# Performance work log

Measured on AMD Instinct MI355X. Metric: run time of the kernel, lower is better.

## Reference

```python
import jax, jax.numpy as jnp
from jax import lax
import numpy as np

B = 8192


def setup_inputs() -> dict:
    key = jax.random.key(0)
    ks = jax.random.split(key, 10)
    rn = lambda i, shape, s: jax.random.normal(ks[i], shape, jnp.float32) * s
    x = jax.random.normal(ks[0], (B, 1, 28, 28), jnp.float32)
    conv1_w = rn(1, (8, 1, 3, 3), 0.3)
    conv2_w = rn(2, (16, 8, 3, 3), 0.15)
    fc1_w = rn(3, (64, 16), 0.25)
    fc2_w = rn(4, (4, 64), 0.15)
    theta = jax.random.uniform(ks[5], (4,), jnp.float32, 0.0, 2.0 * np.pi)
    # RandomLayer (30 random gates) folded into one fixed 16x16 unitary via QR
    a = jax.random.normal(ks[6], (16, 16), jnp.float32)
    b = jax.random.normal(ks[7], (16, 16), jnp.float32)
    q, _ = jnp.linalg.qr((a + 1j * b).astype(jnp.complex64))
    return dict(
        x=x,
        conv1_w=conv1_w, conv1_b=jnp.zeros((8,), jnp.float32),
        conv2_w=conv2_w, conv2_b=jnp.zeros((16,), jnp.float32),
        fc1_w=fc1_w, fc1_b=jnp.zeros((64,), jnp.float32),
        fc2_w=fc2_w, fc2_b=jnp.zeros((4,), jnp.float32),
        norm_g=jnp.ones((4,), jnp.float32), norm_b=jnp.zeros((4,), jnp.float32),
        theta=theta,
        u_re=jnp.real(q).astype(jnp.float32), u_im=jnp.imag(q).astype(jnp.float32),
        qnorm_g=jnp.ones((4,), jnp.float32), qnorm_b=jnp.zeros((4,), jnp.float32),
    )


def _forward(x, conv1_w, conv1_b, conv2_w, conv2_b, fc1_w, fc1_b, fc2_w, fc2_b,
             norm_g, norm_b, theta, u_re, u_im, qnorm_g, qnorm_b):
    bsz = x.shape[0]
    cplx = jnp.complex64

    def conv(h, w, b):
        return lax.conv_general_dilated(h, w, (1, 1), [(1, 1), (1, 1)]) + b[None, :, None, None]

    def mpool(h):
        return lax.reduce_window(h, -jnp.inf, lax.max, (1, 1, 2, 2), (1, 1, 2, 2), 'VALID')

    h = mpool(jax.nn.relu(conv(x, conv1_w, conv1_b)))   # [B,8,14,14]
    h = mpool(jax.nn.relu(conv(h, conv2_w, conv2_b)))   # [B,16,7,7]
    pooled = h[:, :, :6, :6].mean((-1, -2))             # avg_pool2d(.,6) -> [B,16]
    f = jax.nn.relu(pooled @ fc1_w.T + fc1_b)
    out = f @ fc2_w.T + fc2_b                           # [B,4]

    def bn(v, g, b):  # BatchNorm1d, training mode (biased batch var), eps=1e-5
        m = v.mean(0)
        var = v.var(0)
        return g * (v - m) * lax.rsqrt(var + 1e-5) + b

    out = bn(out, norm_g, norm_b)

    # ---- 4-qubit state-vector simulation (wire 0 = most significant bit) ----
    def ry(t):
        c = jnp.cos(t / 2).astype(cplx); s = jnp.sin(t / 2).astype(cplx)
        return jnp.stack([jnp.stack([c, -s], -1), jnp.stack([s, c], -1)], -2)

    def rx(t):
        c = jnp.cos(t / 2).astype(cplx); s = (-1j) * jnp.sin(t / 2).astype(cplx)
        return jnp.stack([jnp.stack([c, s], -1), jnp.stack([s, c], -1)], -2)

    def rz(t):
        e = jnp.exp(-1j * t.astype(cplx) / 2); z = jnp.zeros_like(e)
        return jnp.stack([jnp.stack([e, z], -1), jnp.stack([z, jnp.conj(e)], -1)], -2)

    def ap1(st, U, w):  # apply 1-qubit gate U ([2,2] or [B,2,2]) on wire w
        s = jnp.moveaxis(st, 1 + w, 4)
        sub = 'bxyzi,bji->bxyzj' if U.ndim == 3 else 'bxyzi,ji->bxyzj'
        return jnp.moveaxis(jnp.einsum(sub, s, U), 4, 1 + w)

    def ap_ctrl(st, U, cw, tw):  # controlled-U: ctrl wire cw, target wire tw
        s = jnp.moveaxis(st, (1 + cw, 1 + tw), (3, 4))
        s1 = jnp.einsum('bxyi,ji->bxyj', s[..., 1, :], U)
        s = jnp.stack([s[..., 0, :], s1], axis=-2)
        return jnp.moveaxis(s, (3, 4), (1 + cw, 1 + tw))

    state = jnp.zeros((bsz, 16), cplx).at[:, 0].set(1.0).reshape(bsz, 2, 2, 2, 2)

    # encoder '4x4_ryzxy': RY,RZ,RX,RY rounds over wires 0-3 (4 features cycled)
    ang = jnp.tile(out, (1, 4))  # [B,16]
    enc = [ry] * 4 + [rz] * 4 + [rx] * 4 + [ry] * 4
    for k, fn in enumerate(enc):
        state = ap1(state, fn(ang[:, k]), k % 4)

    # RandomLayer as a fixed 16x16 unitary
    U = (u_re + 1j * u_im).astype(cplx)
    state = jnp.einsum('bi,ji->bj', state.reshape(bsz, 16), U).reshape(bsz, 2, 2, 2, 2)

    state = ap1(state, rx(theta[0]), 0)
    state = ap1(state, ry(theta[1]), 1)
    state = ap1(state, rz(theta[2]), 2)
    state = ap_ctrl(state, rx(theta[3]), 0, 3)
    H = (jnp.array([[1.0, 1.0], [1.0, -1.0]], jnp.float32) / np.float32(np.sqrt(2.0))).astype(cplx)
    SX = 0.5 * jnp.array([[1 + 1j, 1 - 1j], [1 - 1j, 1 + 1j]], cplx)
    X = jnp.array([[0.0, 1.0], [1.0, 0.0]], jnp.float32).astype(cplx)
    state = ap1(state, H, 3)
    state = ap1(state, SX, 2)
    state = ap_ctrl(state, X, 3, 0)

    sf = state.reshape(bsz, 16)
    probs = sf.real ** 2 + sf.imag ** 2                 # [B,16]
    bits = (np.arange(16)[:, None] >> np.arange(3, -1, -1)[None, :]) & 1
    signs = jnp.asarray(1.0 - 2.0 * bits, jnp.float32)  # [16,4] PauliZ eigenvalues per wire
    q_out = probs @ signs                               # [B,4] <Z_w>
    q_out = bn(q_out, qnorm_g, qnorm_b)
    return out + q_out


def reference(x, conv1_w, conv1_b, conv2_w, conv2_b, fc1_w, fc1_b, fc2_w, fc2_b,
              norm_g, norm_b, theta, u_re, u_im, qnorm_g, qnorm_b):
    return _forward(x, conv1_w, conv1_b, conv2_w, conv2_b, fc1_w, fc1_b, fc2_w, fc2_b,
                    norm_g, norm_b, theta, u_re, u_im, qnorm_g, qnorm_b)
```

## Files before the change

### kernel.cpp

```cpp
#include <hip/hip_runtime.h>
#include <math.h>


#define XS_S 34
#define H1_S 20
#define H1_P 280
#define H1I_OFF 9216
#define BT_OFF  13696
#define SMEM_SZ 16000

typedef _Float16 half8 __attribute__((ext_vector_type(8)));
typedef float v4f __attribute__((ext_vector_type(4)));

__device__ __forceinline__ unsigned pkf16(float a, float b) {
    _Float16 ha = (_Float16)a, hb = (_Float16)b;
    unsigned short ua = __builtin_bit_cast(unsigned short, ha);
    unsigned short ub = __builtin_bit_cast(unsigned short, hb);
    return ((unsigned)ub << 16) | (unsigned)ua;
}

__device__ __forceinline__ float2 cmul(float2 a, float2 b) {
    return make_float2(a.x * b.x - a.y * b.y, a.x * b.y + a.y * b.x);
}
__device__ __forceinline__ float2 cadd(float2 a, float2 b) {
    return make_float2(a.x + b.x, a.y + b.y);
}

__device__ __forceinline__ void apply_1q(const float2* src, float2* dst, int t,
                                         float2 g00, float2 g01, float2 g10, float2 g11, int p)
{
    int j = t >> 4, i = t & 15;
    int jb = (j >> p) & 1;
    int k0 = j & ~(1 << p);
    int k1 = j | (1 << p);
    float2 a0 = src[k0 * 16 + i], a1 = src[k1 * 16 + i];
    float2 r = jb ? cadd(cmul(g10, a0), cmul(g11, a1))
                  : cadd(cmul(g00, a0), cmul(g01, a1));
    dst[j * 16 + i] = r;
}

__device__ __forceinline__ void apply_ctrl(const float2* src, float2* dst, int t,
                                           float2 g00, float2 g01, float2 g10, float2 g11,
                                           int pc, int pt)
{
    int j = t >> 4, i = t & 15;
    float2 r;
    if (((j >> pc) & 1) == 0) {
        r = src[j * 16 + i];
    } else {
        int jb = (j >> pt) & 1;
        int k0 = j & ~(1 << pt);
        int k1 = j | (1 << pt);
        float2 a0 = src[k0 * 16 + i], a1 = src[k1 * 16 + i];
        r = jb ? cadd(cmul(g10, a0), cmul(g11, a1))
               : cadd(cmul(g00, a0), cmul(g01, a1));
    }
    dst[j * 16 + i] = r;
}

__global__ __launch_bounds__(256, 6) void k_cnn(
    const float* __restrict__ x,
    const float* __restrict__ w1, const float* __restrict__ b1,
    const float* __restrict__ w2, const float* __restrict__ b2,
    const float* __restrict__ fw1, const float* __restrict__ fb1,
    const float* __restrict__ fw2, const float* __restrict__ fb2,
    float* __restrict__ out_pre, unsigned int* __restrict__ counters)
{
    __shared__ __align__(16) char smem[SMEM_SZ];
    __shared__ float w1t[72];
    __shared__ float b1t[8], b2t[16];
    __shared__ float pool_s[16];

    const int t = threadIdx.x;
    const int b = blockIdx.x;
    const float* xg = x + b * 784;
    float* xs = (float*)smem;
    unsigned* h1u = (unsigned*)(smem + H1I_OFF);

    if (b == 0 && t < 2) counters[t] = 0u;
    if (t < 57) {
        if (t < 29) xs[t] = 0.f;
        else        xs[(t - 28) * XS_S] = 0.f;
    }
    if (t < 108) {
        int pl = t / 27, r = t % 27;
        if (r < 14) h1u[pl * H1_P + r] = 0u;
        else        h1u[pl * H1_P + (r - 13) * H1_S] = 0u;
    }
    if (t >= 64 && t < 136) {
        int i = t - 64;
        w1t[(i % 9) * 8 + (i / 9)] = w1[i];
    }
    if (t < 196) {
        float4 v = ((const float4*)xg)[t];
        int p = t * 4;
        int yy = p / 28, xx = p % 28;
        int base = (yy + 1) * XS_S + xx + 1;
        xs[base] = v.x; xs[base + 1] = v.y; xs[base + 2] = v.z; xs[base + 3] = v.w;
    }
    if (t < 8)  b1t[t] = b1[t];
    if (t < 16) b2t[t] = b2[t];
    __syncthreads();

    if (t < 169) {
        const int py = t / 13, px = t % 13;
        float patch[4][4];
        #pragma unroll
        for (int dr = 0; dr < 4; ++dr) {
            int base = (2 * py + dr) * XS_S + 2 * px;
            float2 a = *(const float2*)&xs[base];
            float2 c = *(const float2*)&xs[base + 2];
            patch[dr][0] = a.x; patch[dr][1] = a.y;
            patch[dr][2] = c.x; patch[dr][3] = c.y;
        }
        float acc[8][2][2];
        #pragma unroll
        for (int c = 0; c < 8; ++c)
            #pragma unroll
            for (int dy = 0; dy < 2; ++dy)
                #pragma unroll
                for (int dx = 0; dx < 2; ++dx) acc[c][dy][dx] = 0.f;
        #pragma unroll
        for (int k = 0; k < 9; ++k) {
            const int ky = k / 3, kx = k % 3;
            float4 wA = *(const float4*)&w1t[k * 8];
            float4 wB = *(const float4*)&w1t[k * 8 + 4];
            float w8[8] = {wA.x, wA.y, wA.z, wA.w, wB.x, wB.y, wB.z, wB.w};
            #pragma unroll
            for (int c = 0; c < 8; ++c)
                #pragma unroll
                for (int dy = 0; dy < 2; ++dy)
                    #pragma unroll
                    for (int dx = 0; dx < 2; ++dx)
                        acc[c][dy][dx] = fmaf(patch[dy + ky][dx + kx], w8[c], acc[c][dy][dx]);
        }
        float v8[8];
        #pragma unroll
        for (int c = 0; c < 8; ++c) {
            float m = fmaxf(fmaxf(acc[c][0][0], acc[c][0][1]),
                            fmaxf(acc[c][1][0], acc[c][1][1])) + b1t[c];
            v8[c] = fmaxf(m, 0.f);
        }
        const int ha = (py + 1) * H1_S + (px + 1);
        h1u[ha]             = pkf16(v8[0], v8[1]);
        h1u[H1_P + ha]      = pkf16(v8[2], v8[3]);
        h1u[2 * H1_P + ha]  = pkf16(v8[4], v8[5]);
        h1u[3 * H1_P + ha]  = pkf16(v8[6], v8[7]);
    } else if (t >= 192) {
        unsigned short* bt = (unsigned short*)(smem + BT_OFF);
        for (int i = t - 192; i < 1152; i += 64) {
            int oc = i / 72, r = i % 72, ic = r / 9, kidx = r % 9;
            _Float16 h = (_Float16)w2[i];
            bt[oc * 72 + kidx * 8 + ic] = __builtin_bit_cast(unsigned short, h);
        }
    }
    __syncthreads();

    const int wv_id = t >> 6, lane = t & 63, quad = lane >> 4, n = lane & 15;
    v4f acc0 = {0.f, 0.f, 0.f, 0.f}, acc1 = acc0, acc2 = acc0;
    if (wv_id < 3) {
        const half8 hz = {0, 0, 0, 0, 0, 0, 0, 0};
        half8 bfr[3];
        int koff[3];
        #pragma unroll
        for (int kc = 0; kc < 3; ++kc) {
            const int kidx = kc * 4 + quad;
            bfr[kc] = (kidx < 9)
                ? *(const half8*)(smem + BT_OFF + n * 144 + kc * 64 + quad * 16)
                : hz;
            koff[kc] = (kidx < 9) ? (kidx / 3) * H1_S + (kidx % 3) : 0;
        }
        #pragma unroll
        for (int g = 0; g < 3; ++g) {
            const int m = (wv_id * 3 + g) * 16 + n;
            const int y = m / 12, xx2 = m % 12;
            const int pbase = y * H1_S + xx2;
            v4f* accp = (g == 0) ? &acc0 : (g == 1) ? &acc1 : &acc2;
            #pragma unroll
            for (int kc = 0; kc < 3; ++kc) {
                const int kidx = kc * 4 + quad;
                half8 af;
                if (kidx < 9) {
                    const int a0 = pbase + koff[kc];
                    uint4 pw;
                    pw.x = h1u[a0];
                    pw.y = h1u[H1_P + a0];
                    pw.z = h1u[2 * H1_P + a0];
                    pw.w = h1u[3 * H1_P + a0];
                    af = __builtin_bit_cast(half8, pw);
                } else {
                    af = hz;
                }
                *accp = __builtin_amdgcn_mfma_f32_16x16x32_f16(af, bfr[kc], *accp, 0, 0, 0);
            }
        }
    }
    __syncthreads();

    float* h2p = (float*)smem;
    if (wv_id < 3) {
        const int posb = (wv_id * 3) * 16 + quad * 4;
        #pragma unroll
        for (int r = 0; r < 4; ++r) h2p[(posb + r) * 16 + n]      = acc0[r];
        #pragma unroll
        for (int r = 0; r < 4; ++r) h2p[(posb + 16 + r) * 16 + n] = acc1[r];
        #pragma unroll
        for (int r = 0; r < 4; ++r) h2p[(posb + 32 + r) * 16 + n] = acc2[r];
    }
    __syncthreads();

    if (t < 64) {
        const int oc = t >> 2, q = t & 3;
        const float bias = b2t[oc];
        float s = 0.f;
        #pragma unroll
        for (int r = 0; r < 9; ++r) {
            int idx = q * 9 + r;
            int pr = idx / 6, pc = idx % 6;
            int p00 = (2 * pr * 12 + 2 * pc) * 16 + oc;
            float m = fmaxf(fmaxf(h2p[p00], h2p[p00 + 16]),
                            fmaxf(h2p[p00 + 192], h2p[p00 + 208]));
            s += fmaxf(m + bias, 0.f);
        }
        s += __shfl_xor(s, 1);
        s += __shfl_xor(s, 2);
        if (q == 0) pool_s[oc] = s * (1.f / 36.f);
    }
    __syncthreads();

    if (t < 64) {
        const float4* f4 = (const float4*)(fw1 + t * 16);
        float4 wa = f4[0], wb = f4[1], wc = f4[2], wd = f4[3];
        float a1 = fb1[t];
        a1 = fmaf(pool_s[0],  wa.x, a1); a1 = fmaf(pool_s[1],  wa.y, a1);
        a1 = fmaf(pool_s[2],  wa.z, a1); a1 = fmaf(pool_s[3],  wa.w, a1);
        a1 = fmaf(pool_s[4],  wb.x, a1); a1 = fmaf(pool_s[5],  wb.y, a1);
        a1 = fmaf(pool_s[6],  wb.z, a1); a1 = fmaf(pool_s[7],  wb.w, a1);
        a1 = fmaf(pool_s[8],  wc.x, a1); a1 = fmaf(pool_s[9],  wc.y, a1);
        a1 = fmaf(pool_s[10], wc.z, a1); a1 = fmaf(pool_s[11], wc.w, a1);
        a1 = fmaf(pool_s[12], wd.x, a1); a1 = fmaf(pool_s[13], wd.y, a1);
        a1 = fmaf(pool_s[14], wd.z, a1); a1 = fmaf(pool_s[15], wd.w, a1);
        float f = fmaxf(a1, 0.f);
        float p0 = f * fw2[t];
        float p1 = f * fw2[64 + t];
        float p2 = f * fw2[128 + t];
        float p3 = f * fw2[192 + t];
        #pragma unroll
        for (int off = 32; off > 0; off >>= 1) {
            p0 += __shfl_down(p0, off);
            p1 += __shfl_down(p1, off);
            p2 += __shfl_down(p2, off);
            p3 += __shfl_down(p3, off);
        }
        if (t == 0) {
            ((float4*)out_pre)[b] = make_float4(p0 + fb2[0], p1 + fb2[1],
                                                p2 + fb2[2], p3 + fb2[3]);
        }
    }
}

__global__ __launch_bounds__(256) void k_tail(
    float* __restrict__ out_pre,
    const float* __restrict__ ng, const float* __restrict__ nb,
    const float* __restrict__ theta,
    const float* __restrict__ u_re, const float* __restrict__ u_im,
    const float* __restrict__ qg, const float* __restrict__ qb,
    float* __restrict__ bins1, float* __restrict__ bins2,
    unsigned int* __restrict__ counters)
{
    __shared__ float red[256];
    __shared__ float ss1[8], ss2[8];
    __shared__ float2 A[256], B[256], Ms[256];
    const int t = threadIdx.x;
    const int sidx = blockIdx.x * 256 + t;

    float4 o4 = ((const float4*)out_pre)[sidx];
    A[t] = make_float2(u_re[t], u_im[t]);
    float th0 = theta[0], th1 = theta[1], th2 = theta[2], th3 = theta[3];

    float vals[8] = {o4.x, o4.y, o4.z, o4.w,
                     o4.x * o4.x, o4.y * o4.y, o4.z * o4.z, o4.w * o4.w};
    #pragma unroll
    for (int off = 32; off > 0; off >>= 1)
        #pragma unroll
        for (int k = 0; k < 8; ++k) vals[k] += __shfl_down(vals[k], off);
    if ((t & 63) == 0) {
        int wid = t >> 6;
        #pragma unroll
        for (int k = 0; k < 8; ++k) red[wid * 8 + k] = vals[k];
    }
    __syncthreads();
    if (t < 8) {
        float s = red[t] + red[8 + t] + red[16 + t] + red[24 + t];
        __hip_atomic_store(&bins1[blockIdx.x * 8 + t], s,
                           __ATOMIC_RELEASE, __HIP_MEMORY_SCOPE_AGENT);
    }
    __syncthreads();
    if (t == 0) { __threadfence(); atomicAdd(&counters[0], 1u); }

    __syncthreads();
    float c0 = cosf(0.5f * th0), s0 = sinf(0.5f * th0);
    apply_1q(A, B, t, make_float2(c0, 0), make_float2(0, -s0),
                      make_float2(0, -s0), make_float2(c0, 0), 3);
    __syncthreads();
    float c1 = cosf(0.5f * th1), s1 = sinf(0.5f * th1);
    apply_1q(B, A, t, make_float2(c1, 0), make_float2(-s1, 0),
                      make_float2(s1, 0), make_float2(c1, 0), 2);
    __syncthreads();
    float c2 = cosf(0.5f * th2), s2 = sinf(0.5f * th2);
    apply_1q(A, B, t, make_float2(c2, -s2), make_float2(0, 0),
                      make_float2(0, 0), make_float2(c2, s2), 1);
    __syncthreads();
    float c3 = cosf(0.5f * th3), s3 = sinf(0.5f * th3);
    apply_ctrl(B, A, t, make_float2(c3, 0), make_float2(0, -s3),
                        make_float2(0, -s3), make_float2(c3, 0), 3, 0);
    __syncthreads();
    const float hh = 0.70710678118654752440f;
    apply_1q(A, B, t, make_float2(hh, 0), make_float2(hh, 0),
                      make_float2(hh, 0), make_float2(-hh, 0), 0);
    __syncthreads();
    apply_1q(B, A, t, make_float2(0.5f, 0.5f), make_float2(0.5f, -0.5f),
                      make_float2(0.5f, -0.5f), make_float2(0.5f, 0.5f), 1);
    __syncthreads();
    apply_ctrl(A, B, t, make_float2(0, 0), make_float2(1, 0),
                        make_float2(1, 0), make_float2(0, 0), 0, 3);
    __syncthreads();
    Ms[t] = B[t];

    if (t == 0) {
        while (__hip_atomic_load(&counters[0], __ATOMIC_ACQUIRE,
                                 __HIP_MEMORY_SCOPE_AGENT) < 32u)
            __builtin_amdgcn_s_sleep(4);
    }
    __syncthreads();
    red[t] = bins1[t];
    __syncthreads();
    if (t < 8) {
        float s = 0.f;
        for (int bb = 0; bb < 32; ++bb) s += red[bb * 8 + t];
        red[t] = s;
    }
    if (t < 4) {
        float mean = red[t] * (1.f / 8192.f);
        float var = red[4 + t] * (1.f / 8192.f) - mean * mean;
        float sc = ng[t] * rsqrtf(var + 1e-5f);
        ss1[t] = sc;
        ss1[4 + t] = nb[t] - mean * sc;
    }
    __syncthreads();

    float a[4];
    a[0] = fmaf(ss1[0], o4.x, ss1[4]);
    a[1] = fmaf(ss1[1], o4.y, ss1[5]);
    a[2] = fmaf(ss1[2], o4.z, ss1[6]);
    a[3] = fmaf(ss1[3], o4.w, ss1[7]);
    float2 v[4][2];
    #pragma unroll
    for (int w = 0; w < 4; ++w) {
        float s, c;
        __sincosf(0.5f * a[w], &s, &c);
        float2 v0 = make_float2(c * c, -c * s);
        float2 v1 = make_float2(s * c, s * s);
        float2 n0 = make_float2(c * v0.x + s * v1.y, c * v0.y - s * v1.x);
        float2 n1 = make_float2(s * v0.y + c * v1.x, -s * v0.x + c * v1.y);
        v[w][0] = make_float2(c * n0.x - s * n1.x, c * n0.y - s * n1.y);
        v[w][1] = make_float2(s * n0.x + c * n1.x, s * n0.y + c * n1.y);
    }
    float2 st[16];
    #pragma unroll
    for (int idx = 0; idx < 16; ++idx) {
        float2 p = cmul(v[0][(idx >> 3) & 1], v[1][(idx >> 2) & 1]);
        p = cmul(p, v[2][(idx >> 1) & 1]);
        st[idx] = cmul(p, v[3][idx & 1]);
    }
    float q[4] = {0.f, 0.f, 0.f, 0.f};
    #pragma unroll
    for (int j = 0; j < 16; ++j) {
        float2 acc = make_float2(0.f, 0.f);
        #pragma unroll
        for (int i = 0; i < 16; ++i) {
            float2 mm = Ms[j * 16 + i];
            acc.x = fmaf(mm.x, st[i].x, acc.x);
            acc.x = fmaf(-mm.y, st[i].y, acc.x);
            acc.y = fmaf(mm.x, st[i].y, acc.y);
            acc.y = fmaf(mm.y, st[i].x, acc.y);
        }
        float pr = acc.x * acc.x + acc.y * acc.y;
        q[0] += ((j >> 3) & 1) ? -pr : pr;
        q[1] += ((j >> 2) & 1) ? -pr : pr;
        q[2] += ((j >> 1) & 1) ? -pr : pr;
        q[3] += (j & 1) ? -pr : pr;
    }

    float vals2[8] = {q[0], q[1], q[2], q[3],
                      q[0] * q[0], q[1] * q[1], q[2] * q[2], q[3] * q[3]};
    #pragma unroll
    for (int off = 32; off > 0; off >>= 1)
        #pragma unroll
        for (int k = 0; k < 8; ++k) vals2[k] += __shfl_down(vals2[k], off);
    __syncthreads();
    if ((t & 63) == 0) {
        int wid = t >> 6;
        #pragma unroll
        for (int k = 0; k < 8; ++k) red[wid * 8 + k] = vals2[k];
    }
    __syncthreads();
    if (t < 8) {
        float s = red[t] + red[8 + t] + red[16 + t] + red[24 + t];
        __hip_atomic_store(&bins2[blockIdx.x * 8 + t], s,
                           __ATOMIC_RELEASE, __HIP_MEMORY_SCOPE_AGENT);
    }
    __syncthreads();
    if (t == 0) {
        __threadfence();
        atomicAdd(&counters[1], 1u);
        while (__hip_atomic_load(&counters[1], __ATOMIC_ACQUIRE,
                                 __HIP_MEMORY_SCOPE_AGENT) < 32u)
            __builtin_amdgcn_s_sleep(4);
    }
    __syncthreads();
    red[t] = bins2[t];
    __syncthreads();
    if (t < 8) {
        float s = 0.f;
        for (int bb = 0; bb < 32; ++bb) s += red[bb * 8 + t];
        red[t] = s;
    }
    if (t < 4) {
        float m2 = red[t] * (1.f / 8192.f);
        float v2 = red[4 + t] * (1.f / 8192.f) - m2 * m2;
        float sc = qg[t] * rsqrtf(v2 + 1e-5f);
        ss2[t] = sc;
        ss2[4 + t] = qb[t] - m2 * sc;
    }
    __syncthreads();

    float4 r;
    r.x = a[0] + fmaf(ss2[0], q[0], ss2[4]);
    r.y = a[1] + fmaf(ss2[1], q[1], ss2[5]);
    r.z = a[2] + fmaf(ss2[2], q[2], ss2[6]);
    r.w = a[3] + fmaf(ss2[3], q[3], ss2[7]);
    ((float4*)out_pre)[sidx] = r;
}

extern "C" void kernel_launch(void* const* d_in, const int* in_sizes, int n_in,
                              void* d_out, int out_size, void* d_ws, size_t ws_size,
                              hipStream_t stream)
{
    const float* x     = (const float*)d_in[0];
    const float* w1    = (const float*)d_in[1];
    const float* b1    = (const float*)d_in[2];
    const float* w2    = (const float*)d_in[3];
    const float* b2    = (const float*)d_in[4];
    const float* fw1   = (const float*)d_in[5];
    const float* fb1   = (const float*)d_in[6];
    const float* fw2   = (const float*)d_in[7];
    const float* fb2   = (const float*)d_in[8];
    const float* ng    = (const float*)d_in[9];
    const float* nb    = (const float*)d_in[10];
    const float* theta = (const float*)d_in[11];
    const float* ure   = (const float*)d_in[12];
    const float* uim   = (const float*)d_in[13];
    const float* qg    = (const float*)d_in[14];
    const float* qb    = (const float*)d_in[15];

    float* ws = (float*)d_ws;
    unsigned int* counters = (unsigned int*)d_ws;
    float* bins1 = ws + 16;
    float* bins2 = ws + 16 + 256;
    float* out_pre = (float*)d_out;

    k_cnn<<<8192, 256, 0, stream>>>(x, w1, b1, w2, b2, fw1, fb1, fw2, fb2,
                                    out_pre, counters);
    k_tail<<<32, 256, 0, stream>>>(out_pre, ng, nb, theta, ure, uim, qg, qb,
                                   bins1, bins2, counters);
}
```

Before: 132.4 us.

## Fuse CNN and tail kernels using last-arriving-block ticket scheme

Merges the per-sample CNN kernel and the batch-norm/quantum tail kernel into one launch. Each block takes a ticket from an atomic counter after writing its output, and the last 32 blocks to finish take over the tail work, spinning until all 8192 blocks are done. This removes the second kernel launch and the gap between kernels. It also drops one barrier between the pooling and FC stages. The cost is a hipMemsetAsync to reset the counters and a spin-wait inside the big grid.

```diff
diff --git a/kernel.cpp b/kernel.cpp
--- a/kernel.cpp
+++ b/kernel.cpp
@@ -58,18 +58,25 @@
     dst[j * 16 + i] = r;
 }
 
-__global__ __launch_bounds__(256, 6) void k_cnn(
+__global__ __launch_bounds__(256, 6) void k_all(
     const float* __restrict__ x,
     const float* __restrict__ w1, const float* __restrict__ b1,
     const float* __restrict__ w2, const float* __restrict__ b2,
     const float* __restrict__ fw1, const float* __restrict__ fb1,
     const float* __restrict__ fw2, const float* __restrict__ fb2,
-    float* __restrict__ out_pre, unsigned int* __restrict__ counters)
+    const float* __restrict__ ng, const float* __restrict__ nb,
+    const float* __restrict__ theta,
+    const float* __restrict__ u_re, const float* __restrict__ u_im,
+    const float* __restrict__ qg, const float* __restrict__ qb,
+    float* __restrict__ out_pre,
+    float* __restrict__ bins1, float* __restrict__ bins2,
+    unsigned int* __restrict__ counters)
 {
     __shared__ __align__(16) char smem[SMEM_SZ];
     __shared__ float w1t[72];
     __shared__ float b1t[8], b2t[16];
     __shared__ float pool_s[16];
+    __shared__ unsigned tick_s;
 
     const int t = threadIdx.x;
     const int b = blockIdx.x;
@@ -77,7 +84,6 @@
     float* xs = (float*)smem;
     unsigned* h1u = (unsigned*)(smem + H1I_OFF);
 
-    if (b == 0 && t < 2) counters[t] = 0u;
     if (t < 57) {
         if (t < 29) xs[t] = 0.f;
         else        xs[(t - 28) * XS_S] = 0.f;
@@ -225,10 +231,7 @@
         s += __shfl_xor(s, 1);
         s += __shfl_xor(s, 2);
         if (q == 0) pool_s[oc] = s * (1.f / 36.f);
-    }
-    __syncthreads();
-
-    if (t < 64) {
+
         const float4* f4 = (const float4*)(fw1 + t * 16);
         float4 wa = f4[0], wb = f4[1], wc = f4[2], wd = f4[3];
         float a1 = fb1[t];
@@ -257,27 +260,64 @@
                                                 p2 + fb2[2], p3 + fb2[3]);
         }
     }
-}
-
-__global__ __launch_bounds__(256) void k_tail(
-    float* __restrict__ out_pre,
-    const float* __restrict__ ng, const float* __restrict__ nb,
-    const float* __restrict__ theta,
-    const float* __restrict__ u_re, const float* __restrict__ u_im,
-    const float* __restrict__ qg, const float* __restrict__ qb,
-    float* __restrict__ bins1, float* __restrict__ bins2,
-    unsigned int* __restrict__ counters)
-{
-    __shared__ float red[256];
+
+    if (t == 0) {
+        __threadfence();
+        tick_s = __hip_atomic_fetch_add(&counters[0], 1u,
+                                        __ATOMIC_ACQ_REL, __HIP_MEMORY_SCOPE_AGENT);
+    }
+    __syncthreads();
+    const unsigned tick = tick_s;
+    if (tick < 8160u) return;
+    const int tb = (int)(tick - 8160u);
+
+    float2* A  = (float2*)smem;
+    float2* B  = (float2*)(smem + 2048);
+    float2* Ms = (float2*)(smem + 4096);
+    float*  red = (float*)(smem + 6144);
     __shared__ float ss1[8], ss2[8];
-    __shared__ float2 A[256], B[256], Ms[256];
-    const int t = threadIdx.x;
-    const int sidx = blockIdx.x * 256 + t;
-
-    float4 o4 = ((const float4*)out_pre)[sidx];
+
     A[t] = make_float2(u_re[t], u_im[t]);
     float th0 = theta[0], th1 = theta[1], th2 = theta[2], th3 = theta[3];
-
+    __syncthreads();
+
+    float c0 = cosf(0.5f * th0), s0 = sinf(0.5f * th0);
+    apply_1q(A, B, t, make_float2(c0, 0), make_float2(0, -s0),
+                      make_float2(0, -s0), make_float2(c0, 0), 3);
+    __syncthreads();
+    float c1 = cosf(0.5f * th1), s1 = sinf(0.5f * th1);
+    apply_1q(B, A, t, make_float2(c1, 0), make_float2(-s1, 0),
+                      make_float2(s1, 0), make_float2(c1, 0), 2);
+    __syncthreads();
+    float c2 = cosf(0.5f * th2), s2 = sinf(0.5f * th2);
+    apply_1q(A, B, t, make_float2(c2, -s2), make_float2(0, 0),
+                      make_float2(0, 0), make_float2(c2, s2), 1);
+    __syncthreads();
+    float c3 = cosf(0.5f * th3), s3 = sinf(0.5f * th3);
+    apply_ctrl(B, A, t, make_float2(c3, 0), make_float2(0, -s3),
+                        make_float2(0, -s3), make_float2(c3, 0), 3, 0);
+    __syncthreads();
+    const float hh = 0.70710678118654752440f;
+    apply_1q(A, B, t, make_float2(hh, 0), make_float2(hh, 0),
+                      make_float2(hh, 0), make_float2(-hh, 0), 0);
+    __syncthreads();
+    apply_1q(B, A, t, make_float2(0.5f, 0.5f), make_float2(0.5f, -0.5f),
+                      make_float2(0.5f, -0.5f), make_float2(0.5f, 0.5f), 1);
+    __syncthreads();
+    apply_ctrl(A, B, t, make_float2(0, 0), make_float2(1, 0),
+                        make_float2(1, 0), make_float2(0, 0), 0, 3);
+    __syncthreads();
+    Ms[t] = B[t];
+
+    if (t == 0) {
+        while (__hip_atomic_load(&counters[0], __ATOMIC_ACQUIRE,
+                                 __HIP_MEMORY_SCOPE_AGENT) < 8192u)
+            __builtin_amdgcn_s_sleep(4);
+    }
+    __syncthreads();
+
+    const int sidx = tb * 256 + t;
+    float4 o4 = ((const float4*)out_pre)[sidx];
     float vals[8] = {o4.x, o4.y, o4.z, o4.w,
                      o4.x * o4.x, o4.y * o4.y, o4.z * o4.z, o4.w * o4.w};
     #pragma unroll
@@ -292,43 +332,14 @@
     __syncthreads();
     if (t < 8) {
         float s = red[t] + red[8 + t] + red[16 + t] + red[24 + t];
-        __hip_atomic_store(&bins1[blockIdx.x * 8 + t], s,
+        __hip_atomic_store(&bins1[tb * 8 + t], s,
                            __ATOMIC_RELEASE, __HIP_MEMORY_SCOPE_AGENT);
     }
     __syncthreads();
-    if (t == 0) { __threadfence(); atomicAdd(&counters[0], 1u); }
-
-    __syncthreads();
-    float c0 = cosf(0.5f * th0), s0 = sinf(0.5f * th0);
-    apply_1q(A, B, t, make_float2(c0, 0), make_float2(0, -s0),
-                      make_float2(0, -s0), make_float2(c0, 0), 3);
-    __syncthreads();
-    float c1 = cosf(0.5f * th1), s1 = sinf(0.5f * th1);
-    apply_1q(B, A, t, make_float2(c1, 0), make_float2(-s1, 0),
-                      make_float2(s1, 0), make_float2(c1, 0), 2);
-    __syncthreads();
-    float c2 = cosf(0.5f * th2), s2 = sinf(0.5f * th2);
-    apply_1q(A, B, t, make_float2(c2, -s2), make_float2(0, 0),
-                      make_float2(0, 0), make_float2(c2, s2), 1);
-    __syncthreads();
-    float c3 = cosf(0.5f * th3), s3 = sinf(0.5f * th3);
-    apply_ctrl(B, A, t, make_float2(c3, 0), make_float2(0, -s3),
-                        make_float2(0, -s3), make_float2(c3, 0), 3, 0);
-    __syncthreads();
-    const float hh = 0.70710678118654752440f;
-    apply_1q(A, B, t, make_float2(hh, 0), make_float2(hh, 0),
-                      make_float2(hh, 0), make_float2(-hh, 0), 0);
-    __syncthreads();
-    apply_1q(B, A, t, make_float2(0.5f, 0.5f), make_float2(0.5f, -0.5f),
-                      make_float2(0.5f, -0.5f), make_float2(0.5f, 0.5f), 1);
-    __syncthreads();
-    apply_ctrl(A, B, t, make_float2(0, 0), make_float2(1, 0),
-                        make_float2(1, 0), make_float2(0, 0), 0, 3);
-    __syncthreads();
-    Ms[t] = B[t];
-
     if (t == 0) {
-        while (__hip_atomic_load(&counters[0], __ATOMIC_ACQUIRE,
+        __threadfence();
+        atomicAdd(&counters[1], 1u);
+        while (__hip_atomic_load(&counters[1], __ATOMIC_ACQUIRE,
                                  __HIP_MEMORY_SCOPE_AGENT) < 32u)
             __builtin_amdgcn_s_sleep(4);
     }
@@ -407,14 +418,14 @@
     __syncthreads();
     if (t < 8) {
         float s = red[t] + red[8 + t] + red[16 + t] + red[24 + t];
-        __hip_atomic_store(&bins2[blockIdx.x * 8 + t], s,
+        __hip_atomic_store(&bins2[tb * 8 + t], s,
                            __ATOMIC_RELEASE, __HIP_MEMORY_SCOPE_AGENT);
     }
     __syncthreads();
     if (t == 0) {
         __threadfence();
-        atomicAdd(&counters[1], 1u);
-        while (__hip_atomic_load(&counters[1], __ATOMIC_ACQUIRE,
+        atomicAdd(&counters[2], 1u);
+        while (__hip_atomic_load(&counters[2], __ATOMIC_ACQUIRE,
                                  __HIP_MEMORY_SCOPE_AGENT) < 32u)
             __builtin_amdgcn_s_sleep(4);
     }
@@ -470,8 +481,8 @@
     float* bins2 = ws + 16 + 256;
     float* out_pre = (float*)d_out;
 
-    k_cnn<<<8192, 256, 0, stream>>>(x, w1, b1, w2, b2, fw1, fb1, fw2, fb2,
-                                    out_pre, counters);
-    k_tail<<<32, 256, 0, stream>>>(out_pre, ng, nb, theta, ure, uim, qg, qb,
-                                   bins1, bins2, counters);
-}
+    hipMemsetAsync(d_ws, 0, 64, stream);
+    k_all<<<8192, 256, 0, stream>>>(x, w1, b1, w2, b2, fw1, fb1, fw2, fb2,
+                                    ng, nb, theta, ure, uim, qg, qb,
+                                    out_pre, bins1, bins2, counters);
+}
```

Result: slower. 474.5 us (+258.3%).
